# Kernel optimization log

Measured on AMD Instinct MI355X. Metric: run time of the kernel, lower is better.

The kernel has to match this reference:

```python
import math
import jax, jax.numpy as jnp
import numpy as np


def _gelu(x):
    return jax.nn.gelu(x, approximate=False)


def _bilinear_sample(feat, gx, gy):
    """grid_sample, mode=bilinear, padding=border, align_corners=True.
    feat: [B,C,H,W]; gx,gy: [B,M] in [-1,1]. Returns [B,M,C]."""
    B, C, H, W = feat.shape
    x = jnp.clip((gx + 1.0) * 0.5 * (W - 1), 0.0, W - 1)
    y = jnp.clip((gy + 1.0) * 0.5 * (H - 1), 0.0, H - 1)
    x0 = jnp.floor(x); y0 = jnp.floor(y)
    wx = (x - x0)[..., None]; wy = (y - y0)[..., None]
    x0i = x0.astype(jnp.int32); y0i = y0.astype(jnp.int32)
    x1i = jnp.minimum(x0i + 1, W - 1); y1i = jnp.minimum(y0i + 1, H - 1)
    ft = jnp.transpose(feat, (0, 2, 3, 1))  # [B,H,W,C]
    gather = jax.vmap(lambda f, yi, xi: f[yi, xi])
    v00 = gather(ft, y0i, x0i); v01 = gather(ft, y0i, x1i)
    v10 = gather(ft, y1i, x0i); v11 = gather(ft, y1i, x1i)
    return (v00 * (1 - wx) * (1 - wy) + v01 * wx * (1 - wy)
            + v10 * (1 - wx) * wy + v11 * wx * wy)


def _layernorm(x, w, b, eps=1e-5):
    m = jnp.mean(x, -1, keepdims=True)
    v = jnp.var(x, -1, keepdims=True)
    return (x - m) / jnp.sqrt(v + eps) * w + b


def _gfb(h, f_next, ph_w, ph_b, gate, w1, b1, w2, b2, ln_w, ln_b):
    g = jax.nn.sigmoid(gate)
    fused = f_next + g * (h @ ph_w + ph_b)
    fused = _gelu(fused @ w1 + b1) @ w2 + b2
    return _layernorm(fused, ln_w, ln_b)


def _forward(img, feat_s8, feat_s16, coarse_flow, query_coords,
             pp_w1, pp_b1, pp_w2, pp_b2, p8_w, p8_b, p16_w, p16_b,
             f1_ph_w, f1_ph_b, f1_gate, f1_w1, f1_b1, f1_w2, f1_b2, f1_ln_w, f1_ln_b,
             f2_ph_w, f2_ph_b, f2_gate, f2_w1, f2_b1, f2_w2, f2_b2, f2_ln_w, f2_ln_b,
             h_w1, h_b1, h_w2, h_b2, h_w3, h_b3):
    B, _, H, W = img.shape
    N = query_coords.shape[1]
    k = 5; half = k // 2
    H8, W8 = coarse_flow.shape[2], coarse_flow.shape[3]
    # normalized grid at query points (x,y)
    gx = 2.0 * query_coords[..., 0] / (W - 1) - 1.0
    gy = 2.0 * query_coords[..., 1] / (H - 1) - 1.0
    coarse_q = _bilinear_sample(coarse_flow, gx, gy)  # [B,N,2]
    coarse_q = coarse_q * jnp.array([W / W8, H / H8], coarse_q.dtype)
    # local k x k RGB patches
    offs = jnp.arange(-half, half + 1, dtype=img.dtype)
    oy, ox = jnp.meshgrid(offs, offs, indexing='ij')
    og = jnp.stack([ox.reshape(-1), oy.reshape(-1)], -1)  # [k*k,2]
    ce = query_coords[:, :, None, :] + og                # [B,N,kk,2]
    pgx = (2.0 * ce[..., 0] / (W - 1) - 1.0).reshape(B, -1)
    pgy = (2.0 * ce[..., 1] / (H - 1) - 1.0).reshape(B, -1)
    patches = _bilinear_sample(img, pgx, pgy).reshape(B, N, k * k * 3)
    f_local = _gelu(patches @ pp_w1 + pp_b1) @ pp_w2 + pp_b2
    f8 = _bilinear_sample(feat_s8, gx, gy) @ p8_w + p8_b
    f16 = _bilinear_sample(feat_s16, gx, gy) @ p16_w + p16_b
    D = f_local.shape[-1]
    h = f_local.reshape(B * N, D)
    h = _gfb(h, f8.reshape(B * N, D), f1_ph_w, f1_ph_b, f1_gate,
             f1_w1, f1_b1, f1_w2, f1_b2, f1_ln_w, f1_ln_b)
    h = _gfb(h, f16.reshape(B * N, D), f2_ph_w, f2_ph_b, f2_gate,
             f2_w1, f2_b1, f2_w2, f2_b2, f2_ln_w, f2_ln_b)
    # relative-in-cell coords + sinusoidal PE (6 bands)
    qx = query_coords[..., 0] / (W / W8)
    qy = query_coords[..., 1] / (H / H8)
    local = jnp.stack([(qx - jnp.round(qx)) * 2.0, (qy - jnp.round(qy)) * 2.0], -1)
    freqs = (2.0 ** jnp.arange(6, dtype=local.dtype)) * math.pi
    xf = local[..., None] * freqs                        # [B,N,2,6]
    enc = jnp.concatenate([jnp.sin(xf), jnp.cos(xf)], -1).reshape(B, N, 24)
    pe = jnp.concatenate([local, enc], -1).reshape(B * N, 26)
    coarse_flat = coarse_q.reshape(B * N, 2)
    mi = jnp.concatenate([h, pe, coarse_flat], -1)       # [B*N, 156]
    delta = _gelu(_gelu(mi @ h_w1 + h_b1) @ h_w2 + h_b2) @ h_w3 + h_b3
    return (coarse_flat + delta).reshape(B, N, 2)


def setup_inputs() -> dict:
    key = jax.random.key(0)
    ks = jax.random.split(key, 40)
    B, H, W = 2, 384, 512
    H8, W8, H16, W16 = 48, 64, 24, 32
    N, D, k = 65536, 128, 5
    pf = 3 * k * k
    def p(i, shape):
        return jax.random.normal(ks[i], shape, jnp.float32) * 0.05
    return {
        'img': jax.random.uniform(ks[0], (B, 3, H, W), jnp.float32),
        'feat_s8': jax.random.normal(ks[1], (B, D, H8, W8), jnp.float32),
        'feat_s16': jax.random.normal(ks[2], (B, D, H16, W16), jnp.float32),
        'coarse_flow': jax.random.normal(ks[3], (B, 2, H8, W8), jnp.float32),
        'query_coords': jax.random.uniform(ks[4], (B, N, 2), jnp.float32)
                        * jnp.array([W - 1.0, H - 1.0], jnp.float32),
        'pp_w1': p(5, (pf, D)), 'pp_b1': p(6, (D,)),
        'pp_w2': p(7, (D, D)), 'pp_b2': p(8, (D,)),
        'p8_w': p(9, (D, D)), 'p8_b': p(10, (D,)),
        'p16_w': p(11, (D, D)), 'p16_b': p(12, (D,)),
        'f1_ph_w': p(13, (D, D)), 'f1_ph_b': p(14, (D,)), 'f1_gate': p(15, (D,)),
        'f1_w1': p(16, (D, 2 * D)), 'f1_b1': p(17, (2 * D,)),
        'f1_w2': p(18, (2 * D, D)), 'f1_b2': p(19, (D,)),
        'f1_ln_w': 1.0 + p(20, (D,)), 'f1_ln_b': p(21, (D,)),
        'f2_ph_w': p(22, (D, D)), 'f2_ph_b': p(23, (D,)), 'f2_gate': p(24, (D,)),
        'f2_w1': p(25, (D, 2 * D)), 'f2_b1': p(26, (2 * D,)),
        'f2_w2': p(27, (2 * D, D)), 'f2_b2': p(28, (D,)),
        'f2_ln_w': 1.0 + p(29, (D,)), 'f2_ln_b': p(30, (D,)),
        'h_w1': p(31, (D + 26 + 2, 128)), 'h_b1': p(32, (128,)),
        'h_w2': p(33, (128, 64)), 'h_b2': p(34, (64,)),
        'h_w3': p(35, (64, 2)), 'h_b3': p(36, (2,)),
    }


def reference(img, feat_s8, feat_s16, coarse_flow, query_coords,
              pp_w1, pp_b1, pp_w2, pp_b2, p8_w, p8_b, p16_w, p16_b,
              f1_ph_w, f1_ph_b, f1_gate, f1_w1, f1_b1, f1_w2, f1_b2, f1_ln_w, f1_ln_b,
              f2_ph_w, f2_ph_b, f2_gate, f2_w1, f2_b1, f2_w2, f2_b2, f2_ln_w, f2_ln_b,
              h_w1, h_b1, h_w2, h_b2, h_w3, h_b3):
    return _forward(img, feat_s8, feat_s16, coarse_flow, query_coords,
                    pp_w1, pp_b1, pp_w2, pp_b2, p8_w, p8_b, p16_w, p16_b,
                    f1_ph_w, f1_ph_b, f1_gate, f1_w1, f1_b1, f1_w2, f1_b2, f1_ln_w, f1_ln_b,
                    f2_ph_w, f2_ph_b, f2_gate, f2_w1, f2_b1, f2_w2, f2_b2, f2_ln_w, f2_ln_b,
                    h_w1, h_b1, h_w2, h_b2, h_w3, h_b3)
```

## Files before the change

kernel.cpp:

```cpp
#include <hip/hip_runtime.h>
#include <math.h>

#define NT 512
#define MB 64
#define MTOT 131072
#define IMG_H 384
#define IMG_W 512
#define H8 48
#define W8 64
#define H16 24
#define W16 32

#define SAB 136
#define SHB 136
#define SPE 40

typedef _Float16 half8_t __attribute__((ext_vector_type(8)));
typedef _Float16 half4_t __attribute__((ext_vector_type(4)));
typedef float f32x4_t __attribute__((ext_vector_type(4)));
typedef unsigned short u16;

#define PW_PP1    0
#define PW_PP2    12288
#define PW_P8CAT  28672
#define PW_P16CAT 61440
#define PW_F1W1   94208
#define PW_F1W2   126976
#define PW_F2W1   159744
#define PW_F2W2   192512
#define PW_HW1    225280
#define PW_HW2    245760
#define PW_END    253952
#define FT8_OFF   PW_END
#define FT8_CNT   (2*H8*W8*128)
#define FT16_OFF  (FT8_OFF + FT8_CNT)
#define FT16_CNT  (2*H16*W16*128)
#define FB_OFF    (FT16_OFF + FT16_CNT)
#define PEG_OFF   (FB_OFF + 512)
#define PEG_CNT   (2048*MB*SPE)
#define CBG_OFF   (PEG_OFF + PEG_CNT)

__device__ __forceinline__ u16 tohalf(float v) {
  return __builtin_bit_cast(u16, (_Float16)v);
}
__device__ __forceinline__ float geluf(float x) {
  float x2 = x * x;
  float t = x * fmaf(x2, 0.0713548162726f, 1.5957691216057308f);
  float e = __expf(-t);
  return x * __builtin_amdgcn_rcpf(1.0f + e);
}

__device__ __forceinline__ float bilin_plane(const float* __restrict__ plane,
                                             int Wd, int Hd, float x, float y) {
  x = fminf(fmaxf(x, 0.f), (float)(Wd - 1));
  y = fminf(fmaxf(y, 0.f), (float)(Hd - 1));
  float x0f = floorf(x), y0f = floorf(y);
  int x0 = (int)x0f, y0 = (int)y0f;
  int x1 = min(x0 + 1, Wd - 1), y1 = min(y0 + 1, Hd - 1);
  float wx = x - x0f, wy = y - y0f;
  const float* r0 = plane + y0 * Wd;
  const float* r1 = plane + y1 * Wd;
  float v00 = r0[x0], v01 = r0[x1], v10 = r1[x0], v11 = r1[x1];
  float top = v00 + wx * (v01 - v00);
  float bot = v10 + wx * (v11 - v10);
  return top + wy * (bot - top);
}

__device__ __forceinline__ void featSample(const u16* __restrict__ ft, int Wd, int Hd,
                                           float x, float y, u16* dstRow, int i16) {
  x = fminf(fmaxf(x, 0.f), (float)(Wd - 1));
  y = fminf(fmaxf(y, 0.f), (float)(Hd - 1));
  float x0f = floorf(x), y0f = floorf(y);
  int x0 = (int)x0f, y0 = (int)y0f;
  int x1 = min(x0 + 1, Wd - 1), y1 = min(y0 + 1, Hd - 1);
  _Float16 wx = (_Float16)(x - x0f), wy = (_Float16)(y - y0f);
  half8_t v00 = *reinterpret_cast<const half8_t*>(ft + (y0 * Wd + x0) * 128 + i16 * 8);
  half8_t v01 = *reinterpret_cast<const half8_t*>(ft + (y0 * Wd + x1) * 128 + i16 * 8);
  half8_t v10 = *reinterpret_cast<const half8_t*>(ft + (y1 * Wd + x0) * 128 + i16 * 8);
  half8_t v11 = *reinterpret_cast<const half8_t*>(ft + (y1 * Wd + x1) * 128 + i16 * 8);
  half8_t top = v00 + wx * (v01 - v00);
  half8_t bot = v10 + wx * (v11 - v10);
  half8_t r = top + wy * (bot - top);
  *reinterpret_cast<half8_t*>(dstRow + i16 * 8) = r;
}

template <int NTW, int KT, int SPLITKT, int ACT, int NWAVES = 8>
__device__ __forceinline__ void mmv(
    const u16* __restrict__ wpk,
    const u16* aA, int strA, const u16* aB, int strB,
    const float* __restrict__ bias,
    u16* oA, int ostrA, u16* oB, int ostrB, int oSplitNt) {
  const int tid = threadIdx.x;
  const int lane = tid & 63;
  const int w = tid >> 6;
  const int l15 = lane & 15;
  const int g = lane >> 4;
  if (NWAVES == 8 || w < NWAVES) {
    f32x4_t acc[NTW][4];
#pragma unroll
    for (int i = 0; i < NTW; ++i)
#pragma unroll
      for (int mt = 0; mt < 4; ++mt) acc[i][mt] = (f32x4_t){0.f, 0.f, 0.f, 0.f};
#pragma unroll
    for (int kt = 0; kt < KT; ++kt) {
      const u16* ab = (kt < SPLITKT) ? (aA + kt * 32) : (aB + (kt - SPLITKT) * 32);
      const int str = (kt < SPLITKT) ? strA : strB;
      half8_t af[4];
#pragma unroll
      for (int mt = 0; mt < 4; ++mt)
        af[mt] = *reinterpret_cast<const half8_t*>(ab + (mt * 16 + l15) * str + g * 8);
#pragma unroll
      for (int i = 0; i < NTW; ++i) {
        const int nt = w + (i << 3);
        half8_t bf = *reinterpret_cast<const half8_t*>(wpk + ((nt * KT + kt) * 64 + lane) * 8);
#pragma unroll
        for (int mt = 0; mt < 4; ++mt)
          acc[i][mt] = __builtin_amdgcn_mfma_f32_16x16x32_f16(bf, af[mt], acc[i][mt], 0, 0, 0);
      }
    }
#pragma unroll
    for (int i = 0; i < NTW; ++i) {
      const int nt = w + (i << 3);
      const int colg = nt << 4;
      f32x4_t bv = *reinterpret_cast<const f32x4_t*>(bias + colg + (g << 2));
      u16* ob; int colB, ostr;
      if (nt < oSplitNt) { ob = oA; colB = colg; ostr = ostrA; }
      else { ob = oB; colB = colg - (oSplitNt << 4); ostr = ostrB; }
#pragma unroll
      for (int mt = 0; mt < 4; ++mt) {
        const int row = (mt << 4) + l15;
        half4_t hv;
#pragma unroll
        for (int r = 0; r < 4; ++r) {
          float v = acc[i][mt][r] + bv[r];
          if (ACT == 1) v = geluf(v);
          hv[r] = (_Float16)v;
        }
        *reinterpret_cast<half4_t*>(ob + row * ostr + colB + (g << 2)) = hv;
      }
    }
  }
}

__device__ __forceinline__ void lnorm(const u16* src, u16* dst,
                                      const float* __restrict__ lw,
                                      const float* __restrict__ lb) {
  const int tid = threadIdx.x;
  int q = tid >> 3, s = tid & 7;
  const u16* rp = src + q * SAB + s * 16;
  float xs[16];
  float sum = 0.f, sum2 = 0.f;
#pragma unroll
  for (int c8 = 0; c8 < 2; ++c8) {
    half8_t v = *reinterpret_cast<const half8_t*>(rp + c8 * 8);
#pragma unroll
    for (int j = 0; j < 8; ++j) {
      float x = (float)v[j];
      xs[c8 * 8 + j] = x; sum += x; sum2 += x * x;
    }
  }
  sum += __shfl_xor(sum, 1); sum2 += __shfl_xor(sum2, 1);
  sum += __shfl_xor(sum, 2); sum2 += __shfl_xor(sum2, 2);
  sum += __shfl_xor(sum, 4); sum2 += __shfl_xor(sum2, 4);
  float mean = sum * 0.0078125f;
  float var = sum2 * 0.0078125f - mean * mean;
  float rstd = rsqrtf(var + 1e-5f);
  u16* op = dst + q * SHB + s * 16;
#pragma unroll
  for (int c8 = 0; c8 < 2; ++c8) {
    half8_t r;
#pragma unroll
    for (int j = 0; j < 8; ++j) {
      int c = s * 16 + c8 * 8 + j;
      r[j] = (_Float16)((xs[c8 * 8 + j] - mean) * rstd * lw[c] + lb[c]);
    }
    *reinterpret_cast<half8_t*>(op + c8 * 8) = r;
  }
}

struct PackArgs {
  const float *pp_w1, *pp_w2, *p8_w, *f1_ph_w, *f1_gate, *p16_w, *f2_ph_w, *f2_gate;
  const float *f1_w1, *f1_w2, *f2_w1, *f2_w2, *h_w1, *h_w2;
  u16* dst;
};

__global__ void pack_weights(PackArgs a) {
  const int KTs[10]   = {3, 4, 8, 8, 4, 8, 4, 8, 5, 4};
  const int Ks[10]    = {75, 128, 256, 256, 128, 256, 128, 256, 156, 128};
  const int bases[11] = {0, 12288, 28672, 61440, 94208, 126976,
                         159744, 192512, 225280, 245760, 253952};
  int stride = gridDim.x * blockDim.x;
  for (int i = blockIdx.x * blockDim.x + threadIdx.x; i < PW_END; i += stride) {
    int s = 0;
    while (i >= bases[s + 1]) ++s;
    int rem = i - bases[s];
    int e = rem & 511, lane = e >> 3, j = e & 7;
    int ntkt = rem >> 9;
    int kt = ntkt % KTs[s], nt = ntkt / KTs[s];
    int k = kt * 32 + ((lane >> 4) << 3) + j;
    int col = (nt << 4) + (lane & 15);
    float v = 0.f;
    if (k < Ks[s]) {
      switch (s) {
        case 0: v = a.pp_w1[k * 128 + col]; break;
        case 1: v = a.pp_w2[k * 128 + col]; break;
        case 2: v = (k < 128) ? a.p8_w[k * 128 + col]
                              : a.f1_ph_w[(k - 128) * 128 + col] /
                                    (1.f + expf(-a.f1_gate[col])); break;
        case 3: v = (k < 128) ? a.p16_w[k * 128 + col]
                              : a.f2_ph_w[(k - 128) * 128 + col] /
                                    (1.f + expf(-a.f2_gate[col])); break;
        case 4: v = a.f1_w1[k * 256 + col]; break;
        case 5: v = a.f1_w2[k * 128 + col]; break;
        case 6: v = a.f2_w1[k * 256 + col]; break;
        case 7: v = a.f2_w2[k * 128 + col]; break;
        case 8: v = a.h_w1[k * 128 + col]; break;
        case 9: v = a.h_w2[k * 64 + col]; break;
      }
    }
    a.dst[i] = tohalf(v);
  }
}

__global__ void fuse_bias(const float* __restrict__ p8_b, const float* __restrict__ f1_ph_b,
                          const float* __restrict__ f1_gate,
                          const float* __restrict__ p16_b, const float* __restrict__ f2_ph_b,
                          const float* __restrict__ f2_gate, float* __restrict__ fb) {
  int t = threadIdx.x;
  if (t < 128) {
    fb[t] = p8_b[t] + f1_ph_b[t] / (1.f + expf(-f1_gate[t]));
    fb[128 + t] = p16_b[t] + f2_ph_b[t] / (1.f + expf(-f2_gate[t]));
  }
}

__global__ void cvt_cl_f16(const float* __restrict__ src, u16* __restrict__ dst,
                           int Hd, int Wd) {
  int total = 2 * 128 * Hd * Wd;
  int stride = gridDim.x * blockDim.x;
  for (int i = blockIdx.x * blockDim.x + threadIdx.x; i < total; i += stride) {
    int x = i % Wd;
    int t = i / Wd;
    int y = t % Hd; t /= Hd;
    int c = t % 128;
    int b = t / 128;
    dst[((b * Hd + y) * Wd + x) * 128 + c] = tohalf(src[i]);
  }
}

struct KParams {
  const float *img, *coarse_flow, *qc;
  const u16 *wpk, *ft8, *ft16;
  const float *fb;
  u16* peg;
  float* cbg;
  const float *pp_b1, *pp_b2;
  const float *f1_b1, *f1_b2, *f1_ln_w, *f1_ln_b;
  const float *f2_b1, *f2_b2, *f2_ln_w, *f2_ln_b;
  const float *h_b1, *h_b2, *h_w3, *h_b3;
  float* out;
};

__global__ __launch_bounds__(NT, 2) void ifd_mfma(KParams P) {
  __shared__ __align__(16) u16 smem[3 * MB * SAB];
  u16* ab0 = smem;
  u16* ab1 = smem + MB * SAB;
  u16* hb  = smem + 2 * MB * SAB;

  const int tid = threadIdx.x;
  const int m0 = blockIdx.x * MB;
  u16* pegB = P.peg + blockIdx.x * (MB * SPE);
  float* cbgB = P.cbg + blockIdx.x * (MB * 2);

  {
    const int q = tid >> 3, sub = tid & 7;
    const int m = m0 + q, b = m >> 16;
    const float qx = P.qc[2 * m], qy = P.qc[2 * m + 1];
    const float* imgb = P.img + b * 3 * (IMG_H * IMG_W);
#pragma unroll
    for (int j = 0; j < 12; ++j) {
      const int c = sub * 12 + j;
      u16 val = 0;
      if (c < 75) {
        int p = c / 3, ch = c - p * 3;
        int iy = p / 5, ix = p - iy * 5;
        val = tohalf(bilin_plane(imgb + ch * (IMG_H * IMG_W), IMG_W, IMG_H,
                                 qx + (float)(ix - 2), qy + (float)(iy - 2)));
      }
      ab0[q * SAB + c] = val;
    }
  }
  if (tid < 128) {
    const int q = tid >> 1, dim = tid & 1;
    const int m = m0 + q;
    const float qv = P.qc[2 * m + dim];
    const float q8 = qv * 0.125f;
    const float loc = (q8 - rintf(q8)) * 2.f;
    pegB[q * SPE + dim] = tohalf(loc);
    const float th = loc * 3.14159265358979323846f;
    float s = __sinf(th), c = __cosf(th);
    const int base = q * SPE + 2 + dim * 12;
#pragma unroll
    for (int bnd = 0; bnd < 6; ++bnd) {
      pegB[base + bnd] = tohalf(s);
      pegB[base + 6 + bnd] = tohalf(c);
      float s2 = 2.f * s * c;
      c = fmaf(-2.f * s, s, 1.f);
      s = s2;
    }
  } else if (tid < 256) {
    const int t2 = tid - 128, q = t2 >> 1, o = t2 & 1;
    const int m = m0 + q, b = m >> 16;
    const float qx = P.qc[2 * m], qy = P.qc[2 * m + 1];
    const float x8 = qx * (63.f / 511.f), y8 = qy * (47.f / 383.f);
    const float cv = 8.f * bilin_plane(P.coarse_flow + (b * 2 + o) * (H8 * W8),
                                       W8, H8, x8, y8);
    pegB[q * SPE + 26 + o] = tohalf(cv);
    cbgB[q * 2 + o] = cv;
  } else if (tid < 384) {
    const int t2 = tid - 256, q = t2 >> 1, pr = t2 & 1;
    *reinterpret_cast<unsigned int*>(pegB + q * SPE + 28 + 2 * pr) = 0u;
  }
  __syncthreads();

  mmv<1, 3, 3, 1>(P.wpk + PW_PP1, ab0, SAB, ab0, SAB, P.pp_b1,
                  ab1, SAB, ab1, SAB, 16);
  __syncthreads();
  mmv<1, 4, 4, 0>(P.wpk + PW_PP2, ab1, SAB, ab1, SAB, P.pp_b2,
                  hb, SHB, hb, SHB, 16);
  for (int i = tid; i < MB * 16; i += NT) {
    int q = i >> 4, i16 = i & 15;
    int m = m0 + q, b = m >> 16;
    float x = P.qc[2 * m] * (63.f / 511.f), y = P.qc[2 * m + 1] * (47.f / 383.f);
    featSample(P.ft8 + b * (H8 * W8 * 128), W8, H8, x, y, ab0 + q * SAB, i16);
  }
  __syncthreads();
  mmv<1, 8, 4, 0>(P.wpk + PW_P8CAT, ab0, SAB, hb, SHB, P.fb,
                  ab1, SAB, ab1, SAB, 16);
  __syncthreads();
  mmv<2, 4, 4, 1>(P.wpk + PW_F1W1, ab1, SAB, ab1, SAB, P.f1_b1,
                  ab0, SAB, hb, SHB, 8);
  __syncthreads();
  mmv<1, 8, 4, 0>(P.wpk + PW_F1W2, ab0, SAB, hb, SHB, P.f1_b2,
                  ab1, SAB, ab1, SAB, 16);
  __syncthreads();
  lnorm(ab1, hb, P.f1_ln_w, P.f1_ln_b);
  for (int i = tid; i < MB * 16; i += NT) {
    int q = i >> 4, i16 = i & 15;
    int m = m0 + q, b = m >> 16;
    float x = P.qc[2 * m] * (31.f / 511.f), y = P.qc[2 * m + 1] * (23.f / 383.f);
    featSample(P.ft16 + b * (H16 * W16 * 128), W16, H16, x, y, ab0 + q * SAB, i16);
  }
  __syncthreads();
  mmv<1, 8, 4, 0>(P.wpk + PW_P16CAT, ab0, SAB, hb, SHB, P.fb + 128,
                  ab1, SAB, ab1, SAB, 16);
  __syncthreads();
  mmv<2, 4, 4, 1>(P.wpk + PW_F2W1, ab1, SAB, ab1, SAB, P.f2_b1,
                  ab0, SAB, hb, SHB, 8);
  __syncthreads();
  mmv<1, 8, 4, 0>(P.wpk + PW_F2W2, ab0, SAB, hb, SHB, P.f2_b2,
                  ab1, SAB, ab1, SAB, 16);
  __syncthreads();
  lnorm(ab1, hb, P.f2_ln_w, P.f2_ln_b);
  __syncthreads();
  mmv<1, 5, 4, 1>(P.wpk + PW_HW1, hb, SHB, pegB, SPE, P.h_b1,
                  ab1, SAB, ab1, SAB, 16);
  __syncthreads();
  mmv<1, 4, 4, 1, 4>(P.wpk + PW_HW2, ab1, SAB, ab1, SAB, P.h_b2,
                     ab0, SAB, ab0, SAB, 16);
  __syncthreads();
  if (tid < 2 * MB) {
    int q = tid >> 1, o = tid & 1;
    float acc = P.h_b3[o];
    const u16* rp = ab0 + q * SAB;
#pragma unroll
    for (int c8 = 0; c8 < 8; ++c8) {
      half8_t v = *reinterpret_cast<const half8_t*>(rp + c8 * 8);
#pragma unroll
      for (int j = 0; j < 8; ++j) acc += (float)v[j] * P.h_w3[(c8 * 8 + j) * 2 + o];
    }
    P.out[(m0 + q) * 2 + o] = cbgB[q * 2 + o] + acc;
  }
}

extern "C" void kernel_launch(void* const* d_in, const int* in_sizes, int n_in,
                              void* d_out, int out_size, void* d_ws, size_t ws_size,
                              hipStream_t stream) {
  u16* wp = (u16*)d_ws;
  float* fb = (float*)(wp + FB_OFF);
  u16* peg = wp + PEG_OFF;
  float* cbg = (float*)(wp + CBG_OFF);

  PackArgs pa;
  pa.pp_w1  = (const float*)d_in[5];
  pa.pp_w2  = (const float*)d_in[7];
  pa.p8_w   = (const float*)d_in[9];
  pa.p16_w  = (const float*)d_in[11];
  pa.f1_ph_w = (const float*)d_in[13];
  pa.f1_gate = (const float*)d_in[15];
  pa.f1_w1  = (const float*)d_in[16];
  pa.f1_w2  = (const float*)d_in[18];
  pa.f2_ph_w = (const float*)d_in[22];
  pa.f2_gate = (const float*)d_in[24];
  pa.f2_w1  = (const float*)d_in[25];
  pa.f2_w2  = (const float*)d_in[27];
  pa.h_w1   = (const float*)d_in[31];
  pa.h_w2   = (const float*)d_in[33];
  pa.dst = wp;
  pack_weights<<<512, 256, 0, stream>>>(pa);
  fuse_bias<<<1, 128, 0, stream>>>((const float*)d_in[10], (const float*)d_in[14],
                                   (const float*)d_in[15], (const float*)d_in[12],
                                   (const float*)d_in[23], (const float*)d_in[24], fb);
  cvt_cl_f16<<<1024, 256, 0, stream>>>((const float*)d_in[1], wp + FT8_OFF, H8, W8);
  cvt_cl_f16<<<256, 256, 0, stream>>>((const float*)d_in[2], wp + FT16_OFF, H16, W16);

  KParams P;
  P.img = (const float*)d_in[0];
  P.coarse_flow = (const float*)d_in[3];
  P.qc = (const float*)d_in[4];
  P.wpk = wp; P.ft8 = wp + FT8_OFF; P.ft16 = wp + FT16_OFF;
  P.fb = fb; P.peg = peg; P.cbg = cbg;
  P.pp_b1 = (const float*)d_in[6];  P.pp_b2 = (const float*)d_in[8];
  P.f1_b1 = (const float*)d_in[17]; P.f1_b2 = (const float*)d_in[19];
  P.f1_ln_w = (const float*)d_in[20]; P.f1_ln_b = (const float*)d_in[21];
  P.f2_b1 = (const float*)d_in[26]; P.f2_b2 = (const float*)d_in[28];
  P.f2_ln_w = (const float*)d_in[29]; P.f2_ln_b = (const float*)d_in[30];
  P.h_b1 = (const float*)d_in[32]; P.h_b2 = (const float*)d_in[34];
  P.h_w3 = (const float*)d_in[35]; P.h_b3 = (const float*)d_in[36];
  P.out = (float*)d_out;

  ifd_mfma<<<MTOT / MB, NT, 0, stream>>>(P);
}
```

Measured before the change: 184.6 us.

## Fold consecutive linear layers into composed weights to remove GEMM stages

Weights of chains of linear layers with no nonlinearity between them (patch MLP second layer, gated projection, feature projection, first fusion MLP layer) are multiplied together in setup kernels. The main kernel then runs one K=256 GEMM per fusion block in place of two or three chained GEMMs, and biases are folded into precomputed vectors. Positional encodings and the coarse flow now stay in shared memory instead of a global scratch buffer. The costs are heavier setup kernels that do O(128) dot products per packed element, larger shared memory that may affect occupancy, and extra fp16 rounding on the composed weights.

Measured after the change: 244.9 us. +32.7%, slower.

```diff
diff --git a/kernel.cpp b/kernel.cpp
--- a/kernel.cpp
+++ b/kernel.cpp
@@ -12,8 +12,7 @@
 #define W16 32
 
 #define SAB 136
-#define SHB 136
-#define SPE 40
+#define SHB 168
 
 typedef _Float16 half8_t __attribute__((ext_vector_type(8)));
 typedef _Float16 half4_t __attribute__((ext_vector_type(4)));
@@ -21,24 +20,18 @@
 typedef unsigned short u16;
 
 #define PW_PP1    0
-#define PW_PP2    12288
-#define PW_P8CAT  28672
-#define PW_P16CAT 61440
-#define PW_F1W1   94208
-#define PW_F1W2   126976
-#define PW_F2W1   159744
-#define PW_F2W2   192512
-#define PW_HW1    225280
-#define PW_HW2    245760
-#define PW_END    253952
+#define PW_MEGA1  12288
+#define PW_S8     77824
+#define PW_MEGA2  110592
+#define PW_S15    176128
+#define PW_HW1    208896
+#define PW_HW2    229376
+#define PW_END    237568
 #define FT8_OFF   PW_END
 #define FT8_CNT   (2*H8*W8*128)
 #define FT16_OFF  (FT8_OFF + FT8_CNT)
 #define FT16_CNT  (2*H16*W16*128)
-#define FB_OFF    (FT16_OFF + FT16_CNT)
-#define PEG_OFF   (FB_OFF + 512)
-#define PEG_CNT   (2048*MB*SPE)
-#define CBG_OFF   (PEG_OFF + PEG_CNT)
+#define F32_OFF   (FT16_OFF + FT16_CNT)
 
 __device__ __forceinline__ u16 tohalf(float v) {
   return __builtin_bit_cast(u16, (_Float16)v);
@@ -178,17 +171,58 @@
   }
 }
 
+__global__ void compose1(const float* __restrict__ pp_w2, const float* __restrict__ f1_ph_w,
+                         const float* __restrict__ f1_gate, const float* __restrict__ f2_ph_w,
+                         const float* __restrict__ f2_gate, const float* __restrict__ p8_b,
+                         const float* __restrict__ f1_ph_b, const float* __restrict__ pp_b2,
+                         float* __restrict__ Wbot1, float* __restrict__ Wph2s,
+                         float* __restrict__ bf1) {
+  int idx = blockIdx.x * blockDim.x + threadIdx.x;
+  if (idx >= 16384) return;
+  int k = idx >> 7, m = idx & 127;
+  float sig1 = 1.f / (1.f + expf(-f1_gate[m]));
+  float acc = 0.f;
+  for (int r = 0; r < 128; ++r) acc += pp_w2[k * 128 + r] * f1_ph_w[r * 128 + m];
+  Wbot1[idx] = acc * sig1;
+  Wph2s[idx] = f2_ph_w[idx] * (1.f / (1.f + expf(-f2_gate[m])));
+  if (k == 0) {
+    float b = 0.f;
+    for (int r = 0; r < 128; ++r) b += pp_b2[r] * f1_ph_w[r * 128 + m];
+    bf1[m] = p8_b[m] + sig1 * f1_ph_b[m] + sig1 * b;
+  }
+}
+
+__global__ void biasAB(const float* __restrict__ bf1, const float* __restrict__ f1_w1,
+                       const float* __restrict__ f1_b1, const float* __restrict__ p16_b,
+                       const float* __restrict__ f2_ph_b, const float* __restrict__ f2_gate,
+                       const float* __restrict__ f2_w1, const float* __restrict__ f2_b1,
+                       float* __restrict__ bA, float* __restrict__ bB) {
+  int n = threadIdx.x;
+  if (n < 256) {
+    float acc = f1_b1[n];
+    for (int m = 0; m < 128; ++m) acc += bf1[m] * f1_w1[m * 256 + n];
+    bA[n] = acc;
+  } else {
+    int n2 = n - 256;
+    float acc = f2_b1[n2];
+    for (int m = 0; m < 128; ++m) {
+      float sig2 = 1.f / (1.f + expf(-f2_gate[m]));
+      acc += (p16_b[m] + sig2 * f2_ph_b[m]) * f2_w1[m * 256 + n2];
+    }
+    bB[n2] = acc;
+  }
+}
+
 struct PackArgs {
-  const float *pp_w1, *pp_w2, *p8_w, *f1_ph_w, *f1_gate, *p16_w, *f2_ph_w, *f2_gate;
-  const float *f1_w1, *f1_w2, *f2_w1, *f2_w2, *h_w1, *h_w2;
+  const float *pp_w1, *p8_w, *f1_w1, *f1_w2, *p16_w, *f2_w1, *f2_w2, *h_w1, *h_w2;
+  const float *Wbot1, *Wph2s;
   u16* dst;
 };
 
 __global__ void pack_weights(PackArgs a) {
-  const int KTs[10]   = {3, 4, 8, 8, 4, 8, 4, 8, 5, 4};
-  const int Ks[10]    = {75, 128, 256, 256, 128, 256, 128, 256, 156, 128};
-  const int bases[11] = {0, 12288, 28672, 61440, 94208, 126976,
-                         159744, 192512, 225280, 245760, 253952};
+  const int KTs[7]   = {3, 8, 8, 8, 8, 5, 4};
+  const int Ks[7]    = {75, 256, 256, 256, 256, 156, 128};
+  const int bases[8] = {0, 12288, 77824, 110592, 176128, 208896, 229376, 237568};
   int stride = gridDim.x * blockDim.x;
   for (int i = blockIdx.x * blockDim.x + threadIdx.x; i < PW_END; i += stride) {
     int s = 0;
@@ -203,33 +237,31 @@
     if (k < Ks[s]) {
       switch (s) {
         case 0: v = a.pp_w1[k * 128 + col]; break;
-        case 1: v = a.pp_w2[k * 128 + col]; break;
-        case 2: v = (k < 128) ? a.p8_w[k * 128 + col]
-                              : a.f1_ph_w[(k - 128) * 128 + col] /
-                                    (1.f + expf(-a.f1_gate[col])); break;
-        case 3: v = (k < 128) ? a.p16_w[k * 128 + col]
-                              : a.f2_ph_w[(k - 128) * 128 + col] /
-                                    (1.f + expf(-a.f2_gate[col])); break;
-        case 4: v = a.f1_w1[k * 256 + col]; break;
-        case 5: v = a.f1_w2[k * 128 + col]; break;
-        case 6: v = a.f2_w1[k * 256 + col]; break;
-        case 7: v = a.f2_w2[k * 128 + col]; break;
-        case 8: v = a.h_w1[k * 128 + col]; break;
-        case 9: v = a.h_w2[k * 64 + col]; break;
+        case 1: {
+          float acc = 0.f;
+          if (k < 128) {
+            for (int m = 0; m < 128; ++m) acc += a.p8_w[k * 128 + m] * a.f1_w1[m * 256 + col];
+          } else {
+            for (int m = 0; m < 128; ++m) acc += a.Wbot1[(k - 128) * 128 + m] * a.f1_w1[m * 256 + col];
+          }
+          v = acc;
+        } break;
+        case 2: v = a.f1_w2[k * 128 + col]; break;
+        case 3: {
+          float acc = 0.f;
+          if (k < 128) {
+            for (int m = 0; m < 128; ++m) acc += a.p16_w[k * 128 + m] * a.f2_w1[m * 256 + col];
+          } else {
+            for (int m = 0; m < 128; ++m) acc += a.Wph2s[(k - 128) * 128 + m] * a.f2_w1[m * 256 + col];
+          }
+          v = acc;
+        } break;
+        case 4: v = a.f2_w2[k * 128 + col]; break;
+        case 5: v = a.h_w1[k * 128 + col]; break;
+        case 6: v = a.h_w2[k * 64 + col]; break;
       }
     }
     a.dst[i] = tohalf(v);
-  }
-}
-
-__global__ void fuse_bias(const float* __restrict__ p8_b, const float* __restrict__ f1_ph_b,
-                          const float* __restrict__ f1_gate,
-                          const float* __restrict__ p16_b, const float* __restrict__ f2_ph_b,
-                          const float* __restrict__ f2_gate, float* __restrict__ fb) {
-  int t = threadIdx.x;
-  if (t < 128) {
-    fb[t] = p8_b[t] + f1_ph_b[t] / (1.f + expf(-f1_gate[t]));
-    fb[128 + t] = p16_b[t] + f2_ph_b[t] / (1.f + expf(-f2_gate[t]));
   }
 }
 
@@ -250,26 +282,24 @@
 struct KParams {
   const float *img, *coarse_flow, *qc;
   const u16 *wpk, *ft8, *ft16;
-  const float *fb;
-  u16* peg;
-  float* cbg;
-  const float *pp_b1, *pp_b2;
-  const float *f1_b1, *f1_b2, *f1_ln_w, *f1_ln_b;
-  const float *f2_b1, *f2_b2, *f2_ln_w, *f2_ln_b;
+  const float *bA, *bB;
+  const float *pp_b1;
+  const float *f1_b2, *f1_ln_w, *f1_ln_b;
+  const float *f2_b2, *f2_ln_w, *f2_ln_b;
   const float *h_b1, *h_b2, *h_w3, *h_b3;
   float* out;
 };
 
 __global__ __launch_bounds__(NT, 2) void ifd_mfma(KParams P) {
-  __shared__ __align__(16) u16 smem[3 * MB * SAB];
+  __shared__ __align__(16) u16 smem[3 * MB * SAB + MB * SHB];
+  __shared__ float cbL[2 * MB];
   u16* ab0 = smem;
   u16* ab1 = smem + MB * SAB;
-  u16* hb  = smem + 2 * MB * SAB;
+  u16* tb  = smem + 2 * MB * SAB;
+  u16* hb  = smem + 3 * MB * SAB;
 
   const int tid = threadIdx.x;
   const int m0 = blockIdx.x * MB;
-  u16* pegB = P.peg + blockIdx.x * (MB * SPE);
-  float* cbgB = P.cbg + blockIdx.x * (MB * 2);
 
   {
     const int q = tid >> 3, sub = tid & 7;
@@ -295,14 +325,14 @@
     const float qv = P.qc[2 * m + dim];
     const float q8 = qv * 0.125f;
     const float loc = (q8 - rintf(q8)) * 2.f;
-    pegB[q * SPE + dim] = tohalf(loc);
+    hb[q * SHB + 128 + dim] = tohalf(loc);
     const float th = loc * 3.14159265358979323846f;
     float s = __sinf(th), c = __cosf(th);
-    const int base = q * SPE + 2 + dim * 12;
+    const int base = q * SHB + 130 + dim * 12;
 #pragma unroll
     for (int bnd = 0; bnd < 6; ++bnd) {
-      pegB[base + bnd] = tohalf(s);
-      pegB[base + 6 + bnd] = tohalf(c);
+      hb[base + bnd] = tohalf(s);
+      hb[base + 6 + bnd] = tohalf(c);
       float s2 = 2.f * s * c;
       c = fmaf(-2.f * s, s, 1.f);
       s = s2;
@@ -314,35 +344,33 @@
     const float x8 = qx * (63.f / 511.f), y8 = qy * (47.f / 383.f);
     const float cv = 8.f * bilin_plane(P.coarse_flow + (b * 2 + o) * (H8 * W8),
                                        W8, H8, x8, y8);
-    pegB[q * SPE + 26 + o] = tohalf(cv);
-    cbgB[q * 2 + o] = cv;
+    hb[q * SHB + 154 + o] = tohalf(cv);
+    cbL[q * 2 + o] = cv;
   } else if (tid < 384) {
     const int t2 = tid - 256, q = t2 >> 1, pr = t2 & 1;
-    *reinterpret_cast<unsigned int*>(pegB + q * SPE + 28 + 2 * pr) = 0u;
+    u16* z = hb + q * SHB + 156 + pr * 6;
+    z[0] = 0; z[1] = 0; z[2] = 0; z[3] = 0; z[4] = 0; z[5] = 0;
   }
   __syncthreads();
 
   mmv<1, 3, 3, 1>(P.wpk + PW_PP1, ab0, SAB, ab0, SAB, P.pp_b1,
                   ab1, SAB, ab1, SAB, 16);
-  __syncthreads();
-  mmv<1, 4, 4, 0>(P.wpk + PW_PP2, ab1, SAB, ab1, SAB, P.pp_b2,
-                  hb, SHB, hb, SHB, 16);
   for (int i = tid; i < MB * 16; i += NT) {
     int q = i >> 4, i16 = i & 15;
     int m = m0 + q, b = m >> 16;
     float x = P.qc[2 * m] * (63.f / 511.f), y = P.qc[2 * m + 1] * (47.f / 383.f);
-    featSample(P.ft8 + b * (H8 * W8 * 128), W8, H8, x, y, ab0 + q * SAB, i16);
-  }
-  __syncthreads();
-  mmv<1, 8, 4, 0>(P.wpk + PW_P8CAT, ab0, SAB, hb, SHB, P.fb,
+    featSample(P.ft8 + b * (H8 * W8 * 128), W8, H8, x, y, hb + q * SHB, i16);
+  }
+  __syncthreads();
+
+  mmv<2, 8, 4, 1>(P.wpk + PW_MEGA1, hb, SHB, ab1, SAB, P.bA,
+                  ab0, SAB, tb, SAB, 8);
+  __syncthreads();
+
+  mmv<1, 8, 4, 0>(P.wpk + PW_S8, ab0, SAB, tb, SAB, P.f1_b2,
                   ab1, SAB, ab1, SAB, 16);
   __syncthreads();
-  mmv<2, 4, 4, 1>(P.wpk + PW_F1W1, ab1, SAB, ab1, SAB, P.f1_b1,
-                  ab0, SAB, hb, SHB, 8);
-  __syncthreads();
-  mmv<1, 8, 4, 0>(P.wpk + PW_F1W2, ab0, SAB, hb, SHB, P.f1_b2,
-                  ab1, SAB, ab1, SAB, 16);
-  __syncthreads();
+
   lnorm(ab1, hb, P.f1_ln_w, P.f1_ln_b);
   for (int i = tid; i < MB * 16; i += NT) {
     int q = i >> 4, i16 = i & 15;
@@ -351,23 +379,26 @@
     featSample(P.ft16 + b * (H16 * W16 * 128), W16, H16, x, y, ab0 + q * SAB, i16);
   }
   __syncthreads();
-  mmv<1, 8, 4, 0>(P.wpk + PW_P16CAT, ab0, SAB, hb, SHB, P.fb + 128,
+
+  mmv<2, 8, 4, 1>(P.wpk + PW_MEGA2, ab0, SAB, hb, SHB, P.bB,
+                  ab1, SAB, tb, SAB, 8);
+  __syncthreads();
+
+  mmv<1, 8, 4, 0>(P.wpk + PW_S15, ab1, SAB, tb, SAB, P.f2_b2,
+                  ab0, SAB, ab0, SAB, 16);
+  __syncthreads();
+
+  lnorm(ab0, hb, P.f2_ln_w, P.f2_ln_b);
+  __syncthreads();
+
+  mmv<1, 5, 5, 1>(P.wpk + PW_HW1, hb, SHB, hb, SHB, P.h_b1,
                   ab1, SAB, ab1, SAB, 16);
   __syncthreads();
-  mmv<2, 4, 4, 1>(P.wpk + PW_F2W1, ab1, SAB, ab1, SAB, P.f2_b1,
-                  ab0, SAB, hb, SHB, 8);
-  __syncthreads();
-  mmv<1, 8, 4, 0>(P.wpk + PW_F2W2, ab0, SAB, hb, SHB, P.f2_b2,
-                  ab1, SAB, ab1, SAB, 16);
-  __syncthreads();
-  lnorm(ab1, hb, P.f2_ln_w, P.f2_ln_b);
-  __syncthreads();
-  mmv<1, 5, 4, 1>(P.wpk + PW_HW1, hb, SHB, pegB, SPE, P.h_b1,
-                  ab1, SAB, ab1, SAB, 16);
-  __syncthreads();
+
   mmv<1, 4, 4, 1, 4>(P.wpk + PW_HW2, ab1, SAB, ab1, SAB, P.h_b2,
                      ab0, SAB, ab0, SAB, 16);
   __syncthreads();
+
   if (tid < 2 * MB) {
     int q = tid >> 1, o = tid & 1;
     float acc = P.h_b3[o];
@@ -378,7 +409,7 @@
 #pragma unroll
       for (int j = 0; j < 8; ++j) acc += (float)v[j] * P.h_w3[(c8 * 8 + j) * 2 + o];
     }
-    P.out[(m0 + q) * 2 + o] = cbgB[q * 2 + o] + acc;
+    P.out[(m0 + q) * 2 + o] = cbL[q * 2 + o] + acc;
   }
 }
 
@@ -386,30 +417,40 @@
                               void* d_out, int out_size, void* d_ws, size_t ws_size,
                               hipStream_t stream) {
   u16* wp = (u16*)d_ws;
-  float* fb = (float*)(wp + FB_OFF);
-  u16* peg = wp + PEG_OFF;
-  float* cbg = (float*)(wp + CBG_OFF);
+  float* fbase = (float*)(wp + F32_OFF);
+  float* Wbot1 = fbase;
+  float* Wph2s = fbase + 16384;
+  float* bf1   = fbase + 32768;
+  float* bA    = fbase + 32896;
+  float* bB    = fbase + 33152;
+
+  const float* pp_w2   = (const float*)d_in[7];
+  const float* f1_ph_w = (const float*)d_in[13];
+  const float* f1_gate = (const float*)d_in[15];
+  const float* f2_ph_w = (const float*)d_in[22];
+  const float* f2_gate = (const float*)d_in[24];
+
+  compose1<<<64, 256, 0, stream>>>(pp_w2, f1_ph_w, f1_gate, f2_ph_w, f2_gate,
+                                   (const float*)d_in[10], (const float*)d_in[14],
+                                   (const float*)d_in[8], Wbot1, Wph2s, bf1);
+  biasAB<<<1, 512, 0, stream>>>(bf1, (const float*)d_in[16], (const float*)d_in[17],
+                                (const float*)d_in[12], (const float*)d_in[23],
+                                f2_gate, (const float*)d_in[25], (const float*)d_in[26],
+                                bA, bB);
 
   PackArgs pa;
-  pa.pp_w1  = (const float*)d_in[5];
-  pa.pp_w2  = (const float*)d_in[7];
-  pa.p8_w   = (const float*)d_in[9];
-  pa.p16_w  = (const float*)d_in[11];
-  pa.f1_ph_w = (const float*)d_in[13];
-  pa.f1_gate = (const float*)d_in[15];
-  pa.f1_w1  = (const float*)d_in[16];
-  pa.f1_w2  = (const float*)d_in[18];
-  pa.f2_ph_w = (const float*)d_in[22];
-  pa.f2_gate = (const float*)d_in[24];
-  pa.f2_w1  = (const float*)d_in[25];
-  pa.f2_w2  = (const float*)d_in[27];
-  pa.h_w1   = (const float*)d_in[31];
-  pa.h_w2   = (const float*)d_in[33];
+  pa.pp_w1 = (const float*)d_in[5];
+  pa.p8_w  = (const float*)d_in[9];
+  pa.f1_w1 = (const float*)d_in[16];
+  pa.f1_w2 = (const float*)d_in[18];
+  pa.p16_w = (const float*)d_in[11];
+  pa.f2_w1 = (const float*)d_in[25];
+  pa.f2_w2 = (const float*)d_in[27];
+  pa.h_w1  = (const float*)d_in[31];
+  pa.h_w2  = (const float*)d_in[33];
+  pa.Wbot1 = Wbot1; pa.Wph2s = Wph2s;
   pa.dst = wp;
-  pack_weights<<<512, 256, 0, stream>>>(pa);
-  fuse_bias<<<1, 128, 0, stream>>>((const float*)d_in[10], (const float*)d_in[14],
-                                   (const float*)d_in[15], (const float*)d_in[12],
-                                   (const float*)d_in[23], (const float*)d_in[24], fb);
+  pack_weights<<<928, 256, 0, stream>>>(pa);
   cvt_cl_f16<<<1024, 256, 0, stream>>>((const float*)d_in[1], wp + FT8_OFF, H8, W8);
   cvt_cl_f16<<<256, 256, 0, stream>>>((const float*)d_in[2], wp + FT16_OFF, H16, W16);
 
@@ -418,11 +459,11 @@
   P.coarse_flow = (const float*)d_in[3];
   P.qc = (const float*)d_in[4];
   P.wpk = wp; P.ft8 = wp + FT8_OFF; P.ft16 = wp + FT16_OFF;
-  P.fb = fb; P.peg = peg; P.cbg = cbg;
-  P.pp_b1 = (const float*)d_in[6];  P.pp_b2 = (const float*)d_in[8];
-  P.f1_b1 = (const float*)d_in[17]; P.f1_b2 = (const float*)d_in[19];
+  P.bA = bA; P.bB = bB;
+  P.pp_b1 = (const float*)d_in[6];
+  P.f1_b2 = (const float*)d_in[19];
   P.f1_ln_w = (const float*)d_in[20]; P.f1_ln_b = (const float*)d_in[21];
-  P.f2_b1 = (const float*)d_in[26]; P.f2_b2 = (const float*)d_in[28];
+  P.f2_b2 = (const float*)d_in[28];
   P.f2_ln_w = (const float*)d_in[29]; P.f2_ln_b = (const float*)d_in[30];
   P.h_b1 = (const float*)d_in[32]; P.h_b2 = (const float*)d_in[34];
   P.h_w3 = (const float*)d_in[35]; P.h_b3 = (const float*)d_in[36];
```
